# Optimization experiments

Hardware: AMD Instinct MI355X
Metric: run time of the kernel (lower is better)

The kernel has to match this reference:

```python
import jax, jax.numpy as jnp
import numpy as np

EMB, HID, V_SRC, V_TGT, NUM_OUT, BOS = 128, 512, 10000, 8000, 9, 0


def _lstm_cell(x, h, c, Wih, Whh, bih, bhh):
    # PyTorch LSTMCell math: gates ordered i, f, g, o
    g = x @ Wih.T + h @ Whh.T + (bih + bhh)
    i, f, gg, o = jnp.split(g, 4, axis=-1)
    i, f, o = jax.nn.sigmoid(i), jax.nn.sigmoid(f), jax.nn.sigmoid(o)
    c = f * c + i * jnp.tanh(gg)
    h = o * jnp.tanh(c)
    return h, c


def setup_inputs() -> dict:
    key = jax.random.key(0)
    ks = jax.random.split(key, 12)
    s = 1.0 / np.sqrt(HID)
    u = lambda k, shp: jax.random.uniform(k, shp, jnp.float32, -s, s)
    src = jax.random.randint(ks[0], (2048, 2), 0, V_SRC)
    src_embed = jax.random.normal(ks[1], (V_SRC, EMB), jnp.float32)
    src_embed = src_embed.at[0].set(0.0)  # padding_idx row
    tgt_embed = jax.random.normal(ks[2], (V_TGT, EMB), jnp.float32)
    tgt_embed = tgt_embed.at[BOS].set(0.0)  # padding_idx=BOS row
    return {
        "src": src,
        "src_embed": src_embed,
        "tgt_embed": tgt_embed,
        "enc_Wih": u(ks[3], (4 * HID, EMB)),
        "enc_Whh": u(ks[4], (4 * HID, HID)),
        "enc_bih": u(ks[5], (4 * HID,)),
        "enc_bhh": u(ks[6], (4 * HID,)),
        "dec_Wih": u(ks[7], (4 * HID, EMB)),
        "dec_Whh": u(ks[8], (4 * HID, HID)),
        "dec_bih": u(ks[9], (4 * HID,)),
        "dec_bhh": u(ks[10], (4 * HID,)),
        "proj_W": u(ks[11], (V_TGT, HID)),
        "proj_b": jnp.zeros((V_TGT,), jnp.float32),
    }


def reference(src, src_embed, tgt_embed, enc_Wih, enc_Whh, enc_bih, enc_bhh,
              dec_Wih, dec_Whh, dec_bih, dec_bhh, proj_W, proj_b):
    B = src.shape[0]
    # ---- encoder over the 2 source tokens ----
    enc_in = src_embed[src]  # (B, 2, EMB); dropout is identity at inference
    h = jnp.zeros((B, HID), jnp.float32)
    c = jnp.zeros((B, HID), jnp.float32)

    def enc_step(carry, x_t):
        h, c = carry
        h, c = _lstm_cell(x_t, h, c, enc_Wih, enc_Whh, enc_bih, enc_bhh)
        return (h, c), None

    (h, c), _ = jax.lax.scan(enc_step, (h, c), jnp.swapaxes(enc_in, 0, 1))

    token0 = jnp.full((B,), BOS, jnp.int32)

    def dec_step(carry, _):
        token, h, c = carry
        x = tgt_embed[token]  # (B, EMB)
        h, c = _lstm_cell(x, h, c, dec_Wih, dec_Whh, dec_bih, dec_bhh)
        logit = h @ proj_W.T + proj_b  # (B, V_TGT)
        nxt = jnp.argmax(logit, axis=-1).astype(jnp.int32)
        return (nxt, h, c), logit

    _, step_logits = jax.lax.scan(dec_step, (token0, h, c), None, length=NUM_OUT)
    # step_logits: (NUM_OUT, B, V_TGT) -> max-pool over steps
    return jnp.max(step_logits, axis=0)
```

## Files before the change

### kernel.cpp

```cpp
#include <hip/hip_runtime.h>
#include <math.h>

#define BB 2048
#define EMB 128
#define HID 512
#define G4 2048
#define VT 8000
#define VTP2 8192
#define NSTEP 9
#define NTILE2 64

typedef short bf16x8 __attribute__((ext_vector_type(8)));
typedef float f32x4 __attribute__((ext_vector_type(4)));

__device__ __forceinline__ ushort f2bf(float x) {
    uint u = __float_as_uint(x);
    uint r = (u + 0x7fffu + ((u >> 16) & 1u)) >> 16;
    return (ushort)r;
}
__device__ __forceinline__ float bf2f(ushort h) {
    return __uint_as_float(((uint)h) << 16);
}
__device__ __forceinline__ float sigm(float x) { return 1.0f / (1.0f + expf(-x)); }

__device__ __forceinline__ void gload16(const ushort* g, ushort* l) {
    __builtin_amdgcn_global_load_lds(
        (const __attribute__((address_space(1))) uint*)g,
        (__attribute__((address_space(3))) uint*)l, 16, 0, 0);
}

__device__ __forceinline__ void stage_tile(
    ushort* Sb,
    const ushort* __restrict__ Ah, const ushort* __restrict__ Al,
    const ushort* __restrict__ Bh, const ushort* __restrict__ Bl,
    int biA, int biB, int K, int k0, int wid, int lane)
{
    const ushort* src = (wid < 2) ? ((wid == 0) ? Ah : Al)
                                  : ((wid == 2) ? Bh : Bl);
    const int rowbase = (wid < 2) ? biA : biB;
    const int rl = lane >> 2, kcp = lane & 3;
    #pragma unroll
    for (int j = 0; j < 8; ++j) {
        int row = j * 16 + rl;
        int kc = (kcp - (row >> 1)) & 3;
        const ushort* g = src + (size_t)(rowbase + row) * K + k0 + kc * 8;
        gload16(g, Sb + wid * 4096 + j * 512);
    }
}

__global__ __launch_bounds__(64) void gather2_kernel(
    ushort* __restrict__ Xhi, ushort* __restrict__ Xlo,
    const float* __restrict__ table,
    const int* __restrict__ src, int mode, int offset,
    const float* __restrict__ partval, const int* __restrict__ partidx)
{
    int row = blockIdx.x, t = threadIdx.x;
    int tok;
    if (mode == 0) {
        tok = src[row * 2 + offset];
    } else if (mode == 1) {
        tok = 0;
    } else {
        float v = partval[(size_t)row * NTILE2 + t];
        int  ix = partidx[(size_t)row * NTILE2 + t];
        #pragma unroll
        for (int off = 1; off < 64; off <<= 1) {
            float ov = __shfl_xor(v, off, 64);
            int   oi = __shfl_xor(ix, off, 64);
            if (ov > v || (ov == v && oi < ix)) { v = ov; ix = oi; }
        }
        tok = ix;
    }
    float2 e = *(const float2*)&table[(size_t)tok * EMB + t * 2];
    ushort2 hh, hl;
    hh.x = f2bf(e.x); hl.x = f2bf(e.x - bf2f(hh.x));
    hh.y = f2bf(e.y); hl.y = f2bf(e.y - bf2f(hh.y));
    *(ushort2*)&Xhi[row * EMB + t * 2] = hh;
    *(ushort2*)&Xlo[row * EMB + t * 2] = hl;
}

__global__ __launch_bounds__(256) void convgate_kernel(
    const float* __restrict__ W, ushort* __restrict__ Whi, ushort* __restrict__ Wlo,
    int kshift)
{
    size_t e0 = ((size_t)blockIdx.x * 256 + threadIdx.x) * 8;
    int K = 1 << kshift;
    int in_row = (int)(e0 >> kshift);
    int q = in_row & 511, gate = in_row >> 9;
    size_t o0 = (((size_t)(q * 4 + gate)) << kshift) + (e0 & (K - 1));
    float4 v0 = *(const float4*)&W[e0];
    float4 v1 = *(const float4*)&W[e0 + 4];
    float x[8] = {v0.x, v0.y, v0.z, v0.w, v1.x, v1.y, v1.z, v1.w};
    uint p[4], qq[4];
    #pragma unroll
    for (int j = 0; j < 4; ++j) {
        ushort h0 = f2bf(x[2 * j]),     l0 = f2bf(x[2 * j] - bf2f(h0));
        ushort h1 = f2bf(x[2 * j + 1]), l1 = f2bf(x[2 * j + 1] - bf2f(h1));
        p[j]  = (uint)h0 | ((uint)h1 << 16);
        qq[j] = (uint)l0 | ((uint)l1 << 16);
    }
    *(uint4*)&Whi[o0] = make_uint4(p[0], p[1], p[2], p[3]);
    *(uint4*)&Wlo[o0] = make_uint4(qq[0], qq[1], qq[2], qq[3]);
}

__global__ __launch_bounds__(256) void convgbias_kernel(
    const float* __restrict__ b0, const float* __restrict__ b1, float* __restrict__ bp)
{
    int i = blockIdx.x * 256 + threadIdx.x;
    int q = i >> 2, gate = i & 3;
    bp[i] = b0[gate * 512 + q] + b1[gate * 512 + q];
}

__global__ __launch_bounds__(256) void convw_kernel(
    const float* __restrict__ W, ushort* __restrict__ Whi, ushort* __restrict__ Wlo)
{
    size_t e0 = ((size_t)blockIdx.x * 256 + threadIdx.x) * 8;
    int row = (int)(e0 >> 9);
    uint p[4], q[4];
    if (row < VT) {
        float4 v0 = *(const float4*)&W[e0];
        float4 v1 = *(const float4*)&W[e0 + 4];
        float x[8] = {v0.x, v0.y, v0.z, v0.w, v1.x, v1.y, v1.z, v1.w};
        #pragma unroll
        for (int j = 0; j < 4; ++j) {
            ushort h0 = f2bf(x[2 * j]),     l0 = f2bf(x[2 * j] - bf2f(h0));
            ushort h1 = f2bf(x[2 * j + 1]), l1 = f2bf(x[2 * j + 1] - bf2f(h1));
            p[j] = (uint)h0 | ((uint)h1 << 16);
            q[j] = (uint)l0 | ((uint)l1 << 16);
        }
    } else {
        #pragma unroll
        for (int j = 0; j < 4; ++j) { p[j] = 0u; q[j] = 0u; }
    }
    *(uint4*)&Whi[e0] = make_uint4(p[0], p[1], p[2], p[3]);
    *(uint4*)&Wlo[e0] = make_uint4(q[0], q[1], q[2], q[3]);
}

__global__ __launch_bounds__(256) void convb_kernel(
    const float* __restrict__ b, float* __restrict__ bp)
{
    int i = blockIdx.x * 256 + threadIdx.x;
    if (i < VTP2) bp[i] = (i < VT) ? b[i] : -1e30f;
}

__global__ __launch_bounds__(256) void gatescell_kernel(
    const ushort* __restrict__ Xhi, const ushort* __restrict__ Xlo,
    const ushort* __restrict__ Hhi, const ushort* __restrict__ Hlo,
    const ushort* __restrict__ WihH, const ushort* __restrict__ WihL,
    const ushort* __restrict__ WhhH, const ushort* __restrict__ WhhL,
    const float* __restrict__ bperm,
    float* __restrict__ Cst,
    ushort* __restrict__ OHhi, ushort* __restrict__ OHlo,
    int nk)
{
    __shared__ ushort S[2][16384];

    const int t = threadIdx.x;
    const int n = blockIdx.x;
    const int tile = (n & 7) * 2 + ((n >> 3) & 1);
    const int rb = n >> 4;
    const int bj0 = tile * 128;
    const int bi0 = rb * 128;
    const int il = t & 15;
    const int g  = (t >> 4) & 3;
    const int wid = t >> 6;
    const int lane = t & 63;
    const int wr = wid >> 1, wc = wid & 1;

    int aofs[4], bofs[4];
    #pragma unroll
    for (int m = 0; m < 4; ++m) {
        int r = wr * 64 + m * 16 + il;
        aofs[m] = r * 32 + (((g + (r >> 1)) & 3) << 3);
    }
    #pragma unroll
    for (int nn = 0; nn < 4; ++nn) {
        int r = wc * 64 + nn * 16 + il;
        bofs[nn] = r * 32 + (((g + (r >> 1)) & 3) << 3);
    }

    f32x4 acc[4][4];
    #pragma unroll
    for (int m = 0; m < 4; ++m)
        #pragma unroll
        for (int nn = 0; nn < 4; ++nn) acc[m][nn] = 0.0f;

    stage_tile(S[0], Xhi, Xlo, WihH, WihL, bi0, bj0, EMB, 0, wid, lane);
    __syncthreads();

    for (int ks = 0; ks < nk; ++ks) {
        int cur = ks & 1;
        if (ks + 1 < nk) {
            int kn = ks + 1;
            if (kn < 4) stage_tile(S[cur ^ 1], Xhi, Xlo, WihH, WihL, bi0, bj0, EMB, kn * 32, wid, lane);
            else        stage_tile(S[cur ^ 1], Hhi, Hlo, WhhH, WhhL, bi0, bj0, HID, (kn - 4) * 32, wid, lane);
        }
        ushort* Sb = S[cur];
        bf16x8 ah[4], al[4];
        #pragma unroll
        for (int m = 0; m < 4; ++m) {
            ah[m] = *(const bf16x8*)&Sb[aofs[m]];
            al[m] = *(const bf16x8*)&Sb[4096 + aofs[m]];
        }
        #pragma unroll
        for (int nn = 0; nn < 4; ++nn) {
            bf16x8 bh = *(const bf16x8*)&Sb[8192 + bofs[nn]];
            bf16x8 bl = *(const bf16x8*)&Sb[12288 + bofs[nn]];
            #pragma unroll
            for (int m = 0; m < 4; ++m) {
                acc[m][nn] = __builtin_amdgcn_mfma_f32_16x16x32_bf16(ah[m], bh, acc[m][nn], 0, 0, 0);
                acc[m][nn] = __builtin_amdgcn_mfma_f32_16x16x32_bf16(ah[m], bl, acc[m][nn], 0, 0, 0);
                acc[m][nn] = __builtin_amdgcn_mfma_f32_16x16x32_bf16(al[m], bh, acc[m][nn], 0, 0, 0);
            }
        }
        __syncthreads();
    }

    float* Tr = (float*)S;
    float bn[4];
    #pragma unroll
    for (int nn = 0; nn < 4; ++nn) bn[nn] = bperm[bj0 + wc * 64 + nn * 16 + il];

    #pragma unroll
    for (int m = 0; m < 4; ++m) {
        #pragma unroll
        for (int nn = 0; nn < 4; ++nn)
            #pragma unroll
            for (int j = 0; j < 4; ++j)
                Tr[(wr * 16 + g * 4 + j) * 132 + wc * 64 + nn * 16 + il] = acc[m][nn][j] + bn[nn];
        __syncthreads();
        #pragma unroll
        for (int it = 0; it < 4; ++it) {
            int lr2 = it * 8 + (t >> 5);
            int c0 = (t & 31) * 4;
            int row = bi0 + m * 16 + ((lr2 >> 4) << 6) + (lr2 & 15);
            int q = (bj0 + c0) >> 2;
            float4 gv = *(float4*)&Tr[lr2 * 132 + c0];
            float gi = sigm(gv.x), gf = sigm(gv.y), gg = tanhf(gv.z), go = sigm(gv.w);
            size_t o = (size_t)row * HID + q;
            float cnew = gf * Cst[o] + gi * gg;
            float h = go * tanhf(cnew);
            Cst[o] = cnew;
            ushort hh = f2bf(h);
            OHhi[o] = hh;
            OHlo[o] = f2bf(h - bf2f(hh));
        }
        __syncthreads();
    }
}

__global__ __launch_bounds__(256) void proj_kernel(
    const ushort* __restrict__ Ahi, const ushort* __restrict__ Alo,
    const ushort* __restrict__ Whi, const ushort* __restrict__ Wlo,
    const float* __restrict__ biasp,
    float* __restrict__ outmax,
    float* __restrict__ partval, int* __restrict__ partidx,
    int mode)
{
    __shared__ ushort S[2][16384];

    const int t = threadIdx.x;
    const int n = blockIdx.x;
    const int xcd = n & 7;
    const int j8 = n >> 3;
    const int tile = xcd * 8 + (j8 & 7);
    const int rb = j8 >> 3;
    const int bj0 = tile * 128;
    const int bi0 = rb * 128;
    const int il = t & 15;
    const int g  = (t >> 4) & 3;
    const int wid = t >> 6;
    const int lane = t & 63;
    const int wr = wid >> 1, wc = wid & 1;

    int aofs[4], bofs[4];
    #pragma unroll
    for (int m = 0; m < 4; ++m) {
        int r = wr * 64 + m * 16 + il;
        aofs[m] = r * 32 + (((g + (r >> 1)) & 3) << 3);
    }
    #pragma unroll
    for (int nn = 0; nn < 4; ++nn) {
        int r = wc * 64 + nn * 16 + il;
        bofs[nn] = r * 32 + (((g + (r >> 1)) & 3) << 3);
    }

    f32x4 acc[4][4];
    #pragma unroll
    for (int m = 0; m < 4; ++m)
        #pragma unroll
        for (int nn = 0; nn < 4; ++nn) acc[m][nn] = 0.0f;

    stage_tile(S[0], Ahi, Alo, Whi, Wlo, bi0, bj0, HID, 0, wid, lane);
    __syncthreads();

    for (int ks = 0; ks < 16; ++ks) {
        int cur = ks & 1;
        if (ks + 1 < 16)
            stage_tile(S[cur ^ 1], Ahi, Alo, Whi, Wlo, bi0, bj0, HID, (ks + 1) * 32, wid, lane);
        ushort* Sb = S[cur];
        bf16x8 ah[4], al[4];
        #pragma unroll
        for (int m = 0; m < 4; ++m) {
            ah[m] = *(const bf16x8*)&Sb[aofs[m]];
            al[m] = *(const bf16x8*)&Sb[4096 + aofs[m]];
        }
        #pragma unroll
        for (int nn = 0; nn < 4; ++nn) {
            bf16x8 bh = *(const bf16x8*)&Sb[8192 + bofs[nn]];
            bf16x8 bl = *(const bf16x8*)&Sb[12288 + bofs[nn]];
            #pragma unroll
            for (int m = 0; m < 4; ++m) {
                acc[m][nn] = __builtin_amdgcn_mfma_f32_16x16x32_bf16(ah[m], bh, acc[m][nn], 0, 0, 0);
                acc[m][nn] = __builtin_amdgcn_mfma_f32_16x16x32_bf16(ah[m], bl, acc[m][nn], 0, 0, 0);
                acc[m][nn] = __builtin_amdgcn_mfma_f32_16x16x32_bf16(al[m], bh, acc[m][nn], 0, 0, 0);
            }
        }
        __syncthreads();
    }

    float* Tr = (float*)S;
    float bn[4];
    #pragma unroll
    for (int nn = 0; nn < 4; ++nn) bn[nn] = biasp[bj0 + wc * 64 + nn * 16 + il];

    #pragma unroll
    for (int m = 0; m < 4; ++m) {
        #pragma unroll
        for (int nn = 0; nn < 4; ++nn)
            #pragma unroll
            for (int j = 0; j < 4; ++j)
                Tr[(wr * 16 + g * 4 + j) * 132 + wc * 64 + nn * 16 + il] = acc[m][nn][j] + bn[nn];
        __syncthreads();
        #pragma unroll
        for (int it = 0; it < 4; ++it) {
            int lr2 = it * 8 + (t >> 5);
            int c0 = (t & 31) * 4;
            int row = bi0 + m * 16 + ((lr2 >> 4) << 6) + (lr2 & 15);
            int col = bj0 + c0;
            float4 cur = *(float4*)&Tr[lr2 * 132 + c0];

            float bv = cur.x; int bix = col;
            if (cur.y > bv) { bv = cur.y; bix = col + 1; }
            if (cur.z > bv) { bv = cur.z; bix = col + 2; }
            if (cur.w > bv) { bv = cur.w; bix = col + 3; }
            #pragma unroll
            for (int off = 1; off < 32; off <<= 1) {
                float ov = __shfl_xor(bv, off, 64);
                int   oi = __shfl_xor(bix, off, 64);
                if (ov > bv || (ov == bv && oi < bix)) { bv = ov; bix = oi; }
            }
            if ((t & 31) == 0) {
                partval[(size_t)row * NTILE2 + tile] = bv;
                partidx[(size_t)row * NTILE2 + tile] = bix;
            }

            if (col < VT) {
                float* op = &outmax[(size_t)row * VT + col];
                float4 o = cur;
                if (mode == 2) {
                    float4 p = *(const float4*)op;
                    o.x = fmaxf(o.x, p.x); o.y = fmaxf(o.y, p.y);
                    o.z = fmaxf(o.z, p.z); o.w = fmaxf(o.w, p.w);
                }
                *(float4*)op = o;
            }
        }
        __syncthreads();
    }
}

extern "C" void kernel_launch(void* const* d_in, const int* in_sizes, int n_in,
                              void* d_out, int out_size, void* d_ws, size_t ws_size,
                              hipStream_t stream) {
    const int*   src       = (const int*)d_in[0];
    const float* src_embed = (const float*)d_in[1];
    const float* tgt_embed = (const float*)d_in[2];
    const float* enc_Wih   = (const float*)d_in[3];
    const float* enc_Whh   = (const float*)d_in[4];
    const float* enc_bih   = (const float*)d_in[5];
    const float* enc_bhh   = (const float*)d_in[6];
    const float* dec_Wih   = (const float*)d_in[7];
    const float* dec_Whh   = (const float*)d_in[8];
    const float* dec_bih   = (const float*)d_in[9];
    const float* dec_bhh   = (const float*)d_in[10];
    const float* proj_W    = (const float*)d_in[11];
    const float* proj_b    = (const float*)d_in[12];
    float* out = (float*)d_out;

    char* ws = (char*)d_ws;
    float*  C     = (float*)ws;   ws += (size_t)BB * HID * 4;
    float*  PV    = (float*)ws;   ws += (size_t)BB * NTILE2 * 4;
    int*    PI    = (int*)ws;     ws += (size_t)BB * NTILE2 * 4;
    ushort* Xhi   = (ushort*)ws;  ws += (size_t)BB * EMB * 2;
    ushort* Xlo   = (ushort*)ws;  ws += (size_t)BB * EMB * 2;
    ushort* Hhi   = (ushort*)ws;  ws += (size_t)BB * HID * 2;
    ushort* Hlo   = (ushort*)ws;  ws += (size_t)BB * HID * 2;
    ushort* PWhi  = (ushort*)ws;  ws += (size_t)VTP2 * HID * 2;
    ushort* PWlo  = (ushort*)ws;  ws += (size_t)VTP2 * HID * 2;
    float*  biasp = (float*)ws;   ws += (size_t)VTP2 * 4;
    ushort* eWihH = (ushort*)ws;  ws += (size_t)G4 * EMB * 2;
    ushort* eWihL = (ushort*)ws;  ws += (size_t)G4 * EMB * 2;
    ushort* eWhhH = (ushort*)ws;  ws += (size_t)G4 * HID * 2;
    ushort* eWhhL = (ushort*)ws;  ws += (size_t)G4 * HID * 2;
    ushort* dWihH = (ushort*)ws;  ws += (size_t)G4 * EMB * 2;
    ushort* dWihL = (ushort*)ws;  ws += (size_t)G4 * EMB * 2;
    ushort* dWhhH = (ushort*)ws;  ws += (size_t)G4 * HID * 2;
    ushort* dWhhL = (ushort*)ws;  ws += (size_t)G4 * HID * 2;
    float*  BSe   = (float*)ws;   ws += (size_t)G4 * 4;
    float*  BSd   = (float*)ws;   ws += (size_t)G4 * 4;

    hipMemsetAsync(C, 0, (size_t)BB * HID * 4, stream);

    convw_kernel<<<VTP2 * HID / 8 / 256, 256, 0, stream>>>(proj_W, PWhi, PWlo);
    convb_kernel<<<VTP2 / 256, 256, 0, stream>>>(proj_b, biasp);
    convgate_kernel<<<G4 * EMB / 8 / 256, 256, 0, stream>>>(enc_Wih, eWihH, eWihL, 7);
    convgate_kernel<<<G4 * HID / 8 / 256, 256, 0, stream>>>(enc_Whh, eWhhH, eWhhL, 9);
    convgate_kernel<<<G4 * EMB / 8 / 256, 256, 0, stream>>>(dec_Wih, dWihH, dWihL, 7);
    convgate_kernel<<<G4 * HID / 8 / 256, 256, 0, stream>>>(dec_Whh, dWhhH, dWhhL, 9);
    convgbias_kernel<<<G4 / 256, 256, 0, stream>>>(enc_bih, enc_bhh, BSe);
    convgbias_kernel<<<G4 / 256, 256, 0, stream>>>(dec_bih, dec_bhh, BSd);

    for (int tstep = 0; tstep < 2; ++tstep) {
        gather2_kernel<<<BB, 64, 0, stream>>>(Xhi, Xlo, src_embed, src, 0, tstep, PV, PI);
        gatescell_kernel<<<256, 256, 0, stream>>>(Xhi, Xlo, Hhi, Hlo,
            eWihH, eWihL, eWhhH, eWhhL, BSe, C, Hhi, Hlo, tstep == 0 ? 4 : 20);
    }

    for (int s = 0; s < NSTEP; ++s) {
        gather2_kernel<<<BB, 64, 0, stream>>>(Xhi, Xlo, tgt_embed, nullptr,
            (s == 0 ? 1 : 2), 0, PV, PI);
        gatescell_kernel<<<256, 256, 0, stream>>>(Xhi, Xlo, Hhi, Hlo,
            dWihH, dWihL, dWhhH, dWhhL, BSd, C, Hhi, Hlo, 20);
        proj_kernel<<<1024, 256, 0, stream>>>(Hhi, Hlo, PWhi, PWlo, biasp,
            out, PV, PI, (s == 0 ? 1 : 2));
    }
}
```

Measured before the change: 1.120 ms.

## Widen projection GEMM tile to 128x256 with triple-buffered LDS pipeline

```diff
diff --git a/kernel.cpp b/kernel.cpp
--- a/kernel.cpp
+++ b/kernel.cpp
@@ -8,7 +8,7 @@
 #define VT 8000
 #define VTP2 8192
 #define NSTEP 9
-#define NTILE2 64
+#define PT 32
 
 typedef short bf16x8 __attribute__((ext_vector_type(8)));
 typedef float f32x4 __attribute__((ext_vector_type(4)));
@@ -45,6 +45,27 @@
         int kc = (kcp - (row >> 1)) & 3;
         const ushort* g = src + (size_t)(rowbase + row) * K + k0 + kc * 8;
         gload16(g, Sb + wid * 4096 + j * 512);
+    }
+}
+
+__device__ __forceinline__ void stage3(
+    ushort* Sb,
+    const ushort* __restrict__ Ah, const ushort* __restrict__ Al,
+    const ushort* __restrict__ Bh, const ushort* __restrict__ Bl,
+    int biA, int biB, int k0, int wid, int lane)
+{
+    const int rl = lane >> 2, kcp = lane & 3;
+    #pragma unroll
+    for (int j = 0; j < 6; ++j) {
+        int c = wid * 6 + j;
+        const ushort* src;
+        int row, base;
+        if (c < 8)       { src = Ah; row = c * 16 + rl;        base = biA; }
+        else if (c < 16) { src = Al; row = (c - 8) * 16 + rl;  base = biA; }
+        else if (c < 32) { src = Bh; row = (c - 16) * 16 + rl; base = biB; }
+        else             { src = Bl; row = (c - 32) * 16 + rl; base = biB; }
+        int kc = (kcp - (row >> 1)) & 3;
+        gload16(src + (size_t)(base + row) * HID + k0 + kc * 8, Sb + c * 512);
     }
 }
 
@@ -61,8 +82,8 @@
     } else if (mode == 1) {
         tok = 0;
     } else {
-        float v = partval[(size_t)row * NTILE2 + t];
-        int  ix = partidx[(size_t)row * NTILE2 + t];
+        float v = (t < PT) ? partval[(size_t)row * PT + t] : -INFINITY;
+        int  ix = (t < PT) ? partidx[(size_t)row * PT + t] : 0x7fffffff;
         #pragma unroll
         for (int off = 1; off < 64; off <<= 1) {
             float ov = __shfl_xor(v, off, 64);
@@ -249,7 +270,7 @@
     }
 }
 
-__global__ __launch_bounds__(256) void proj_kernel(
+__global__ __launch_bounds__(512, 1) void proj_kernel(
     const ushort* __restrict__ Ahi, const ushort* __restrict__ Alo,
     const ushort* __restrict__ Whi, const ushort* __restrict__ Wlo,
     const float* __restrict__ biasp,
@@ -257,21 +278,22 @@
     float* __restrict__ partval, int* __restrict__ partidx,
     int mode)
 {
-    __shared__ ushort S[2][16384];
+    __shared__ ushort S[3][24576];
 
     const int t = threadIdx.x;
     const int n = blockIdx.x;
     const int xcd = n & 7;
-    const int j8 = n >> 3;
-    const int tile = xcd * 8 + (j8 & 7);
-    const int rb = j8 >> 3;
-    const int bj0 = tile * 128;
+    const int q8 = n >> 3;
+    const int tile = xcd * 4 + (q8 & 3);
+    const int rb = q8 >> 2;
+    const int bj0 = tile * 256;
     const int bi0 = rb * 128;
+    const int lane = t & 63;
+    const int wid = t >> 6;
     const int il = t & 15;
     const int g  = (t >> 4) & 3;
-    const int wid = t >> 6;
-    const int lane = t & 63;
-    const int wr = wid >> 1, wc = wid & 1;
+    const int wr = wid >> 2;
+    const int wc = wid & 3;
 
     int aofs[4], bofs[4];
     #pragma unroll
@@ -282,7 +304,7 @@
     #pragma unroll
     for (int nn = 0; nn < 4; ++nn) {
         int r = wc * 64 + nn * 16 + il;
-        bofs[nn] = r * 32 + (((g + (r >> 1)) & 3) << 3);
+        bofs[nn] = 8192 + r * 32 + (((g + (r >> 1)) & 3) << 3);
     }
 
     f32x4 acc[4][4];
@@ -291,15 +313,23 @@
         #pragma unroll
         for (int nn = 0; nn < 4; ++nn) acc[m][nn] = 0.0f;
 
-    stage_tile(S[0], Ahi, Alo, Whi, Wlo, bi0, bj0, HID, 0, wid, lane);
-    __syncthreads();
-
+    stage3(S[0], Ahi, Alo, Whi, Wlo, bi0, bj0, 0,  wid, lane);
+    stage3(S[1], Ahi, Alo, Whi, Wlo, bi0, bj0, 32, wid, lane);
+
+    #pragma unroll 1
     for (int ks = 0; ks < 16; ++ks) {
-        int cur = ks & 1;
-        if (ks + 1 < 16)
-            stage_tile(S[cur ^ 1], Ahi, Alo, Whi, Wlo, bi0, bj0, HID, (ks + 1) * 32, wid, lane);
-        ushort* Sb = S[cur];
-        bf16x8 ah[4], al[4];
+        __builtin_amdgcn_sched_barrier(0);
+        if (ks + 2 < 16)
+            stage3(S[(ks + 2) % 3], Ahi, Alo, Whi, Wlo, bi0, bj0, (ks + 2) * 32, wid, lane);
+        __builtin_amdgcn_sched_barrier(0);
+        if (ks + 2 < 16)      asm volatile("s_waitcnt vmcnt(12)" ::: "memory");
+        else if (ks + 1 < 16) asm volatile("s_waitcnt vmcnt(6)" ::: "memory");
+        else                  asm volatile("s_waitcnt vmcnt(0)" ::: "memory");
+        __builtin_amdgcn_s_barrier();
+        __builtin_amdgcn_sched_barrier(0);
+
+        const ushort* Sb = S[ks % 3];
+        bf16x8 ah[4], al[4], bh[4], bl[4];
         #pragma unroll
         for (int m = 0; m < 4; ++m) {
             ah[m] = *(const bf16x8*)&Sb[aofs[m]];
@@ -307,16 +337,22 @@
         }
         #pragma unroll
         for (int nn = 0; nn < 4; ++nn) {
-            bf16x8 bh = *(const bf16x8*)&Sb[8192 + bofs[nn]];
-            bf16x8 bl = *(const bf16x8*)&Sb[12288 + bofs[nn]];
+            bh[nn] = *(const bf16x8*)&Sb[bofs[nn]];
+            bl[nn] = *(const bf16x8*)&Sb[8192 + bofs[nn]];
+        }
+        __builtin_amdgcn_s_setprio(1);
+        #pragma unroll
+        for (int nn = 0; nn < 4; ++nn) {
             #pragma unroll
             for (int m = 0; m < 4; ++m) {
-                acc[m][nn] = __builtin_amdgcn_mfma_f32_16x16x32_bf16(ah[m], bh, acc[m][nn], 0, 0, 0);
-                acc[m][nn] = __builtin_amdgcn_mfma_f32_16x16x32_bf16(ah[m], bl, acc[m][nn], 0, 0, 0);
-                acc[m][nn] = __builtin_amdgcn_mfma_f32_16x16x32_bf16(al[m], bh, acc[m][nn], 0, 0, 0);
+                acc[m][nn] = __builtin_amdgcn_mfma_f32_16x16x32_bf16(ah[m], bh[nn], acc[m][nn], 0, 0, 0);
+                acc[m][nn] = __builtin_amdgcn_mfma_f32_16x16x32_bf16(ah[m], bl[nn], acc[m][nn], 0, 0, 0);
+                acc[m][nn] = __builtin_amdgcn_mfma_f32_16x16x32_bf16(al[m], bh[nn], acc[m][nn], 0, 0, 0);
             }
         }
-        __syncthreads();
+        __builtin_amdgcn_s_setprio(0);
+        __builtin_amdgcn_sched_barrier(0);
+        __builtin_amdgcn_s_barrier();
     }
 
     float* Tr = (float*)S;
@@ -330,29 +366,29 @@
         for (int nn = 0; nn < 4; ++nn)
             #pragma unroll
             for (int j = 0; j < 4; ++j)
-                Tr[(wr * 16 + g * 4 + j) * 132 + wc * 64 + nn * 16 + il] = acc[m][nn][j] + bn[nn];
+                Tr[(wr * 16 + g * 4 + j) * 260 + wc * 64 + nn * 16 + il] = acc[m][nn][j] + bn[nn];
         __syncthreads();
         #pragma unroll
         for (int it = 0; it < 4; ++it) {
-            int lr2 = it * 8 + (t >> 5);
-            int c0 = (t & 31) * 4;
+            int lr2 = it * 8 + wid;
+            int c0 = lane * 4;
             int row = bi0 + m * 16 + ((lr2 >> 4) << 6) + (lr2 & 15);
             int col = bj0 + c0;
-            float4 cur = *(float4*)&Tr[lr2 * 132 + c0];
+            float4 cur = *(float4*)&Tr[lr2 * 260 + c0];
 
             float bv = cur.x; int bix = col;
             if (cur.y > bv) { bv = cur.y; bix = col + 1; }
             if (cur.z > bv) { bv = cur.z; bix = col + 2; }
             if (cur.w > bv) { bv = cur.w; bix = col + 3; }
             #pragma unroll
-            for (int off = 1; off < 32; off <<= 1) {
+            for (int off = 1; off < 64; off <<= 1) {
                 float ov = __shfl_xor(bv, off, 64);
                 int   oi = __shfl_xor(bix, off, 64);
                 if (ov > bv || (ov == bv && oi < bix)) { bv = ov; bix = oi; }
             }
-            if ((t & 31) == 0) {
-                partval[(size_t)row * NTILE2 + tile] = bv;
-                partidx[(size_t)row * NTILE2 + tile] = bix;
+            if (lane == 0) {
+                partval[(size_t)row * PT + tile] = bv;
+                partidx[(size_t)row * PT + tile] = bix;
             }
 
             if (col < VT) {
@@ -390,8 +426,8 @@
 
     char* ws = (char*)d_ws;
     float*  C     = (float*)ws;   ws += (size_t)BB * HID * 4;
-    float*  PV    = (float*)ws;   ws += (size_t)BB * NTILE2 * 4;
-    int*    PI    = (int*)ws;     ws += (size_t)BB * NTILE2 * 4;
+    float*  PV    = (float*)ws;   ws += (size_t)BB * PT * 4;
+    int*    PI    = (int*)ws;     ws += (size_t)BB * PT * 4;
     ushort* Xhi   = (ushort*)ws;  ws += (size_t)BB * EMB * 2;
     ushort* Xlo   = (ushort*)ws;  ws += (size_t)BB * EMB * 2;
     ushort* Hhi   = (ushort*)ws;  ws += (size_t)BB * HID * 2;
@@ -432,7 +468,7 @@
             (s == 0 ? 1 : 2), 0, PV, PI);
         gatescell_kernel<<<256, 256, 0, stream>>>(Xhi, Xlo, Hhi, Hlo,
             dWihH, dWihL, dWhhH, dWhhL, BSd, C, Hhi, Hlo, 20);
-        proj_kernel<<<1024, 256, 0, stream>>>(Hhi, Hlo, PWhi, PWlo, biasp,
+        proj_kernel<<<512, 512, 0, stream>>>(Hhi, Hlo, PWhi, PWlo, biasp,
             out, PV, PI, (s == 0 ? 1 : 2));
     }
 }
```

New measurement: 1.132 ms. About the same (+1.1%).

## Use 8 waves in gates kernel and single-pass epilogue via full-tile LDS transpose

Applied to the files above, without the earlier changes.

```diff
diff --git a/kernel.cpp b/kernel.cpp
--- a/kernel.cpp
+++ b/kernel.cpp
@@ -9,6 +9,7 @@
 #define VTP2 8192
 #define NSTEP 9
 #define NTILE2 64
+#define LDW 132
 
 typedef short bf16x8 __attribute__((ext_vector_type(8)));
 typedef float f32x4 __attribute__((ext_vector_type(4)));
@@ -29,7 +30,7 @@
         (__attribute__((address_space(3))) uint*)l, 16, 0, 0);
 }
 
-__device__ __forceinline__ void stage_tile(
+__device__ __forceinline__ void stage4(
     ushort* Sb,
     const ushort* __restrict__ Ah, const ushort* __restrict__ Al,
     const ushort* __restrict__ Bh, const ushort* __restrict__ Bl,
@@ -45,6 +46,28 @@
         int kc = (kcp - (row >> 1)) & 3;
         const ushort* g = src + (size_t)(rowbase + row) * K + k0 + kc * 8;
         gload16(g, Sb + wid * 4096 + j * 512);
+    }
+}
+
+__device__ __forceinline__ void stage8(
+    ushort* Sb,
+    const ushort* __restrict__ Ah, const ushort* __restrict__ Al,
+    const ushort* __restrict__ Bh, const ushort* __restrict__ Bl,
+    int biA, int biB, int K, int k0, int wid, int lane)
+{
+    const int rl = lane >> 2, kcp = lane & 3;
+    #pragma unroll
+    for (int j = 0; j < 4; ++j) {
+        int c = wid * 4 + j;
+        int region = c >> 3;
+        int rowblk = c & 7;
+        int row = rowblk * 16 + rl;
+        int kc = (kcp - (row >> 1)) & 3;
+        const ushort* src = (region < 2) ? (region == 0 ? Ah : Al)
+                                         : (region == 2 ? Bh : Bl);
+        int base = (region < 2) ? biA : biB;
+        gload16(src + (size_t)(base + row) * K + k0 + kc * 8,
+                Sb + region * 4096 + rowblk * 512);
     }
 }
 
@@ -143,7 +166,7 @@
     if (i < VTP2) bp[i] = (i < VT) ? b[i] : -1e30f;
 }
 
-__global__ __launch_bounds__(256) void gatescell_kernel(
+__global__ __launch_bounds__(512) void gatescell_kernel(
     const ushort* __restrict__ Xhi, const ushort* __restrict__ Xlo,
     const ushort* __restrict__ Hhi, const ushort* __restrict__ Hlo,
     const ushort* __restrict__ WihH, const ushort* __restrict__ WihL,
@@ -153,7 +176,8 @@
     ushort* __restrict__ OHhi, ushort* __restrict__ OHlo,
     int nk)
 {
-    __shared__ ushort S[2][16384];
+    __shared__ __align__(16) char smem[128 * LDW * 4];
+    ushort* S0 = (ushort*)smem;
 
     const int t = threadIdx.x;
     const int n = blockIdx.x;
@@ -165,37 +189,38 @@
     const int g  = (t >> 4) & 3;
     const int wid = t >> 6;
     const int lane = t & 63;
-    const int wr = wid >> 1, wc = wid & 1;
-
-    int aofs[4], bofs[4];
+    const int wr = wid >> 2;
+    const int wc = wid & 3;
+
+    int aofs[4], bofs[2];
     #pragma unroll
     for (int m = 0; m < 4; ++m) {
         int r = wr * 64 + m * 16 + il;
         aofs[m] = r * 32 + (((g + (r >> 1)) & 3) << 3);
     }
     #pragma unroll
-    for (int nn = 0; nn < 4; ++nn) {
-        int r = wc * 64 + nn * 16 + il;
-        bofs[nn] = r * 32 + (((g + (r >> 1)) & 3) << 3);
-    }
-
-    f32x4 acc[4][4];
+    for (int nn = 0; nn < 2; ++nn) {
+        int r = wc * 32 + nn * 16 + il;
+        bofs[nn] = 8192 + r * 32 + (((g + (r >> 1)) & 3) << 3);
+    }
+
+    f32x4 acc[4][2];
     #pragma unroll
     for (int m = 0; m < 4; ++m)
         #pragma unroll
-        for (int nn = 0; nn < 4; ++nn) acc[m][nn] = 0.0f;
-
-    stage_tile(S[0], Xhi, Xlo, WihH, WihL, bi0, bj0, EMB, 0, wid, lane);
+        for (int nn = 0; nn < 2; ++nn) acc[m][nn] = 0.0f;
+
+    stage8(S0, Xhi, Xlo, WihH, WihL, bi0, bj0, EMB, 0, wid, lane);
     __syncthreads();
 
     for (int ks = 0; ks < nk; ++ks) {
         int cur = ks & 1;
         if (ks + 1 < nk) {
             int kn = ks + 1;
-            if (kn < 4) stage_tile(S[cur ^ 1], Xhi, Xlo, WihH, WihL, bi0, bj0, EMB, kn * 32, wid, lane);
-            else        stage_tile(S[cur ^ 1], Hhi, Hlo, WhhH, WhhL, bi0, bj0, HID, (kn - 4) * 32, wid, lane);
-        }
-        ushort* Sb = S[cur];
+            if (kn < 4) stage8(S0 + (cur ^ 1) * 16384, Xhi, Xlo, WihH, WihL, bi0, bj0, EMB, kn * 32, wid, lane);
+            else        stage8(S0 + (cur ^ 1) * 16384, Hhi, Hlo, WhhH, WhhL, bi0, bj0, HID, (kn - 4) * 32, wid, lane);
+        }
+        ushort* Sb = S0 + cur * 16384;
         bf16x8 ah[4], al[4];
         #pragma unroll
         for (int m = 0; m < 4; ++m) {
@@ -203,9 +228,9 @@
             al[m] = *(const bf16x8*)&Sb[4096 + aofs[m]];
         }
         #pragma unroll
-        for (int nn = 0; nn < 4; ++nn) {
-            bf16x8 bh = *(const bf16x8*)&Sb[8192 + bofs[nn]];
-            bf16x8 bl = *(const bf16x8*)&Sb[12288 + bofs[nn]];
+        for (int nn = 0; nn < 2; ++nn) {
+            bf16x8 bh = *(const bf16x8*)&Sb[bofs[nn]];
+            bf16x8 bl = *(const bf16x8*)&Sb[4096 + bofs[nn]];
             #pragma unroll
             for (int m = 0; m < 4; ++m) {
                 acc[m][nn] = __builtin_amdgcn_mfma_f32_16x16x32_bf16(ah[m], bh, acc[m][nn], 0, 0, 0);
@@ -216,36 +241,34 @@
         __syncthreads();
     }
 
-    float* Tr = (float*)S;
-    float bn[4];
-    #pragma unroll
-    for (int nn = 0; nn < 4; ++nn) bn[nn] = bperm[bj0 + wc * 64 + nn * 16 + il];
-
-    #pragma unroll
-    for (int m = 0; m < 4; ++m) {
-        #pragma unroll
-        for (int nn = 0; nn < 4; ++nn)
+    float* Tr = (float*)smem;
+    float bn[2];
+    #pragma unroll
+    for (int nn = 0; nn < 2; ++nn) bn[nn] = bperm[bj0 + wc * 32 + nn * 16 + il];
+
+    #pragma unroll
+    for (int m = 0; m < 4; ++m)
+        #pragma unroll
+        for (int nn = 0; nn < 2; ++nn)
             #pragma unroll
             for (int j = 0; j < 4; ++j)
-                Tr[(wr * 16 + g * 4 + j) * 132 + wc * 64 + nn * 16 + il] = acc[m][nn][j] + bn[nn];
-        __syncthreads();
-        #pragma unroll
-        for (int it = 0; it < 4; ++it) {
-            int lr2 = it * 8 + (t >> 5);
-            int c0 = (t & 31) * 4;
-            int row = bi0 + m * 16 + ((lr2 >> 4) << 6) + (lr2 & 15);
-            int q = (bj0 + c0) >> 2;
-            float4 gv = *(float4*)&Tr[lr2 * 132 + c0];
-            float gi = sigm(gv.x), gf = sigm(gv.y), gg = tanhf(gv.z), go = sigm(gv.w);
-            size_t o = (size_t)row * HID + q;
-            float cnew = gf * Cst[o] + gi * gg;
-            float h = go * tanhf(cnew);
-            Cst[o] = cnew;
-            ushort hh = f2bf(h);
-            OHhi[o] = hh;
-            OHlo[o] = f2bf(h - bf2f(hh));
-        }
-        __syncthreads();
+                Tr[(wr * 64 + m * 16 + g * 4 + j) * LDW + wc * 32 + nn * 16 + il]
+                    = acc[m][nn][j] + bn[nn];
+    __syncthreads();
+
+    #pragma unroll
+    for (int it = 0; it < 8; ++it) {
+        int row = it * 16 + (t >> 5);
+        int c4 = t & 31;
+        float4 gv = *(float4*)&Tr[row * LDW + c4 * 4];
+        float gi = sigm(gv.x), gf = sigm(gv.y), gg = tanhf(gv.z), go = sigm(gv.w);
+        size_t o = (size_t)(bi0 + row) * HID + (bj0 >> 2) + c4;
+        float cnew = gf * Cst[o] + gi * gg;
+        float h = go * tanhf(cnew);
+        Cst[o] = cnew;
+        ushort hh = f2bf(h);
+        OHhi[o] = hh;
+        OHlo[o] = f2bf(h - bf2f(hh));
     }
 }
 
@@ -257,7 +280,8 @@
     float* __restrict__ partval, int* __restrict__ partidx,
     int mode)
 {
-    __shared__ ushort S[2][16384];
+    __shared__ __align__(16) char smem[128 * LDW * 4];
+    ushort* S0 = (ushort*)smem;
 
     const int t = threadIdx.x;
     const int n = blockIdx.x;
@@ -282,7 +306,7 @@
     #pragma unroll
     for (int nn = 0; nn < 4; ++nn) {
         int r = wc * 64 + nn * 16 + il;
-        bofs[nn] = r * 32 + (((g + (r >> 1)) & 3) << 3);
+        bofs[nn] = 8192 + r * 32 + (((g + (r >> 1)) & 3) << 3);
     }
 
     f32x4 acc[4][4];
@@ -291,14 +315,14 @@
         #pragma unroll
         for (int nn = 0; nn < 4; ++nn) acc[m][nn] = 0.0f;
 
-    stage_tile(S[0], Ahi, Alo, Whi, Wlo, bi0, bj0, HID, 0, wid, lane);
+    stage4(S0, Ahi, Alo, Whi, Wlo, bi0, bj0, HID, 0, wid, lane);
     __syncthreads();
 
     for (int ks = 0; ks < 16; ++ks) {
         int cur = ks & 1;
         if (ks + 1 < 16)
-            stage_tile(S[cur ^ 1], Ahi, Alo, Whi, Wlo, bi0, bj0, HID, (ks + 1) * 32, wid, lane);
-        ushort* Sb = S[cur];
+            stage4(S0 + (cur ^ 1) * 16384, Ahi, Alo, Whi, Wlo, bi0, bj0, HID, (ks + 1) * 32, wid, lane);
+        ushort* Sb = S0 + cur * 16384;
         bf16x8 ah[4], al[4];
         #pragma unroll
         for (int m = 0; m < 4; ++m) {
@@ -307,8 +331,8 @@
         }
         #pragma unroll
         for (int nn = 0; nn < 4; ++nn) {
-            bf16x8 bh = *(const bf16x8*)&Sb[8192 + bofs[nn]];
-            bf16x8 bl = *(const bf16x8*)&Sb[12288 + bofs[nn]];
+            bf16x8 bh = *(const bf16x8*)&Sb[bofs[nn]];
+            bf16x8 bl = *(const bf16x8*)&Sb[4096 + bofs[nn]];
             #pragma unroll
             for (int m = 0; m < 4; ++m) {
                 acc[m][nn] = __builtin_amdgcn_mfma_f32_16x16x32_bf16(ah[m], bh, acc[m][nn], 0, 0, 0);
@@ -319,54 +343,54 @@
         __syncthreads();
     }
 
-    float* Tr = (float*)S;
+    float* Tr = (float*)smem;
     float bn[4];
     #pragma unroll
     for (int nn = 0; nn < 4; ++nn) bn[nn] = biasp[bj0 + wc * 64 + nn * 16 + il];
 
     #pragma unroll
-    for (int m = 0; m < 4; ++m) {
+    for (int m = 0; m < 4; ++m)
         #pragma unroll
         for (int nn = 0; nn < 4; ++nn)
             #pragma unroll
             for (int j = 0; j < 4; ++j)
-                Tr[(wr * 16 + g * 4 + j) * 132 + wc * 64 + nn * 16 + il] = acc[m][nn][j] + bn[nn];
-        __syncthreads();
-        #pragma unroll
-        for (int it = 0; it < 4; ++it) {
-            int lr2 = it * 8 + (t >> 5);
-            int c0 = (t & 31) * 4;
-            int row = bi0 + m * 16 + ((lr2 >> 4) << 6) + (lr2 & 15);
-            int col = bj0 + c0;
-            float4 cur = *(float4*)&Tr[lr2 * 132 + c0];
-
-            float bv = cur.x; int bix = col;
-            if (cur.y > bv) { bv = cur.y; bix = col + 1; }
-            if (cur.z > bv) { bv = cur.z; bix = col + 2; }
-            if (cur.w > bv) { bv = cur.w; bix = col + 3; }
-            #pragma unroll
-            for (int off = 1; off < 32; off <<= 1) {
-                float ov = __shfl_xor(bv, off, 64);
-                int   oi = __shfl_xor(bix, off, 64);
-                if (ov > bv || (ov == bv && oi < bix)) { bv = ov; bix = oi; }
+                Tr[(wr * 64 + m * 16 + g * 4 + j) * LDW + wc * 64 + nn * 16 + il]
+                    = acc[m][nn][j] + bn[nn];
+    __syncthreads();
+
+    #pragma unroll
+    for (int it = 0; it < 16; ++it) {
+        int row2 = it * 8 + (t >> 5);
+        int c4 = t & 31;
+        int row = bi0 + row2;
+        int col = bj0 + c4 * 4;
+        float4 cur = *(float4*)&Tr[row2 * LDW + c4 * 4];
+
+        float bv = cur.x; int bix = col;
+        if (cur.y > bv) { bv = cur.y; bix = col + 1; }
+        if (cur.z > bv) { bv = cur.z; bix = col + 2; }
+        if (cur.w > bv) { bv = cur.w; bix = col + 3; }
+        #pragma unroll
+        for (int off = 1; off < 32; off <<= 1) {
+            float ov = __shfl_xor(bv, off, 64);
+            int   oi = __shfl_xor(bix, off, 64);
+            if (ov > bv || (ov == bv && oi < bix)) { bv = ov; bix = oi; }
+        }
+        if ((t & 31) == 0) {
+            partval[(size_t)row * NTILE2 + tile] = bv;
+            partidx[(size_t)row * NTILE2 + tile] = bix;
+        }
+
+        if (col < VT) {
+            float* op = &outmax[(size_t)row * VT + col];
+            float4 o = cur;
+            if (mode == 2) {
+                float4 p = *(const float4*)op;
+                o.x = fmaxf(o.x, p.x); o.y = fmaxf(o.y, p.y);
+                o.z = fmaxf(o.z, p.z); o.w = fmaxf(o.w, p.w);
             }
-            if ((t & 31) == 0) {
-                partval[(size_t)row * NTILE2 + tile] = bv;
-                partidx[(size_t)row * NTILE2 + tile] = bix;
-            }
-
-            if (col < VT) {
-                float* op = &outmax[(size_t)row * VT + col];
-                float4 o = cur;
-                if (mode == 2) {
-                    float4 p = *(const float4*)op;
-                    o.x = fmaxf(o.x, p.x); o.y = fmaxf(o.y, p.y);
-                    o.z = fmaxf(o.z, p.z); o.w = fmaxf(o.w, p.w);
-                }
-                *(float4*)op = o;
-            }
-        }
-        __syncthreads();
+            *(float4*)op = o;
+        }
     }
 }
 
@@ -423,14 +447,14 @@
 
     for (int tstep = 0; tstep < 2; ++tstep) {
         gather2_kernel<<<BB, 64, 0, stream>>>(Xhi, Xlo, src_embed, src, 0, tstep, PV, PI);
-        gatescell_kernel<<<256, 256, 0, stream>>>(Xhi, Xlo, Hhi, Hlo,
+        gatescell_kernel<<<256, 512, 0, stream>>>(Xhi, Xlo, Hhi, Hlo,
             eWihH, eWihL, eWhhH, eWhhL, BSe, C, Hhi, Hlo, tstep == 0 ? 4 : 20);
     }
 
     for (int s = 0; s < NSTEP; ++s) {
         gather2_kernel<<<BB, 64, 0, stream>>>(Xhi, Xlo, tgt_embed, nullptr,
             (s == 0 ? 1 : 2), 0, PV, PI);
-        gatescell_kernel<<<256, 256, 0, stream>>>(Xhi, Xlo, Hhi, Hlo,
+        gatescell_kernel<<<256, 512, 0, stream>>>(Xhi, Xlo, Hhi, Hlo,
             dWihH, dWihL, dWhhH, dWhhL, BSd, C, Hhi, Hlo, 20);
         proj_kernel<<<1024, 256, 0, stream>>>(Hhi, Hlo, PWhi, PWlo, biasp,
             out, PV, PI, (s == 0 ? 1 : 2));
```

Measured after the change: 1.089 ms. 2.7% less time.
